# Kernel tuning notes

Measured on AMD Instinct MI355X. Metric: run time of the kernel, lower is better.

The kernel has to match this reference:

```python
import jax, jax.numpy as jnp
import numpy as np

NUM_NODES = 116
EMBED = 64
HIDDEN = 64
OUT_FEAT = 116


def mish(x):
    return x * jnp.tanh(jax.nn.softplus(x))


def sage_conv(x, src, dst, w_l, b_l, w_r, n):
    # PyG SAGEConv (mean aggr): out = lin_l(mean_{j->i} x_j) + lin_r(x_i)
    agg = jax.ops.segment_sum(x[src], dst, num_segments=n)
    cnt = jax.ops.segment_sum(jnp.ones((src.shape[0],), x.dtype), dst, num_segments=n)
    mean = agg / jnp.clip(cnt, 1.0)[:, None]
    return mean @ w_l.T + b_l + x @ w_r.T


def setup_inputs() -> dict:
    key = jax.random.key(0)
    ks = jax.random.split(key, 12)
    B = 64
    N = B * NUM_NODES          # 7424 total nodes
    E = N * 32                 # 237568 edges
    d_in = EMBED * NUM_NODES   # 7424
    d_hid = HIDDEN * NUM_NODES # 7424
    d_out = OUT_FEAT * NUM_NODES  # 13456

    def lin_w(k, fan_out, fan_in):
        s = 1.0 / np.sqrt(fan_in)
        return jax.random.uniform(k, (fan_out, fan_in), jnp.float32, -s, s)

    return {
        "z": jax.random.normal(ks[0], (N, EMBED), jnp.float32),
        "edge_index": jax.random.randint(ks[1], (2, E), 0, N, jnp.int64),
        "batch_size": B,
        "w1_l": lin_w(ks[2], EMBED, EMBED),
        "b1_l": jnp.zeros((EMBED,), jnp.float32),
        "w1_r": lin_w(ks[3], EMBED, EMBED),
        "w2_l": lin_w(ks[4], EMBED, EMBED),
        "b2_l": jnp.zeros((EMBED,), jnp.float32),
        "w2_r": lin_w(ks[5], EMBED, EMBED),
        "fc1_w": lin_w(ks[6], d_hid, d_in),
        "fc1_b": jax.random.uniform(ks[7], (d_hid,), jnp.float32, -1/np.sqrt(d_in), 1/np.sqrt(d_in)),
        "fc2_w": lin_w(ks[8], d_out, d_hid),
        "fc2_b": jax.random.uniform(ks[9], (d_out,), jnp.float32, -1/np.sqrt(d_hid), 1/np.sqrt(d_hid)),
    }


def reference(z, edge_index, batch_size, w1_l, b1_l, w1_r, w2_l, b2_l, w2_r,
              fc1_w, fc1_b, fc2_w, fc2_b):
    n = z.shape[0]
    src, dst = edge_index[0], edge_index[1]
    h = mish(sage_conv(z, src, dst, w1_l, b1_l, w1_r, n))
    h = mish(sage_conv(h, src, dst, w2_l, b2_l, w2_r, n))
    h_flat = h.reshape(batch_size, NUM_NODES * EMBED)
    hidden = mish(h_flat @ fc1_w.T + fc1_b)
    x_rec = (hidden @ fc2_w.T + fc2_b).reshape(batch_size, NUM_NODES, OUT_FEAT)
    # enforce symmetry, unit diagonal
    sym = 0.5 * (x_rec + jnp.swapaxes(x_rec, 1, 2))
    eye = jnp.eye(NUM_NODES, dtype=bool)[None]
    sym = jnp.where(eye, jnp.asarray(1.0, sym.dtype), sym)
    return sym.reshape(batch_size * NUM_NODES, OUT_FEAT)
```

## Files before the change

kernel.cpp:

```cpp
#include <hip/hip_runtime.h>
#include <math.h>

#define NODES_TOT 7424
#define EDGES     237568
#define BATCH     64
#define NN        116
#define KDIM      7424
#define N1        7424
#define N2        13456
#define NKB       116
#define KSPLIT    8

typedef __attribute__((ext_vector_type(8))) short bf16x8;
typedef __attribute__((ext_vector_type(4))) float f32x4;
typedef __attribute__((ext_vector_type(4))) short s16x4;

__device__ __forceinline__ float mish_f(float v) {
    float sp = fmaxf(v, 0.0f) + log1pf(expf(-fabsf(v)));
    return v * tanhf(sp);
}

__device__ __forceinline__ unsigned short bf_rne(float f) {
    unsigned u = __float_as_uint(f);
    u += 0x7fffu + ((u >> 16) & 1u);
    return (unsigned short)(u >> 16);
}

__device__ __forceinline__ void gload_lds16(const void* g, void* l) {
    __builtin_amdgcn_global_load_lds(
        (const __attribute__((address_space(1))) void*)g,
        (__attribute__((address_space(3))) void*)l, 16, 0, 0);
}

__global__ void zero_kernel(int* __restrict__ p, int n) {
    int i = blockIdx.x * 256 + threadIdx.x;
    if (i < n) p[i] = 0;
}

__global__ void hist_kernel(const int* __restrict__ dst, int* __restrict__ hist) {
    int e = blockIdx.x * 256 + threadIdx.x;
    if (e < EDGES) atomicAdd(&hist[dst[e]], 1);
}

__global__ void scan_kernel(const int* __restrict__ hist, int* __restrict__ row_start,
                            int* __restrict__ cursor) {
    __shared__ int s[1024];
    int t = threadIdx.x;
    int base = t * 8;
    int loc[8];
    int sum = 0;
    #pragma unroll
    for (int c = 0; c < 8; ++c) {
        int idx = base + c;
        int v = (idx < NODES_TOT) ? hist[idx] : 0;
        loc[c] = sum;
        sum += v;
    }
    s[t] = sum;
    __syncthreads();
    for (int off = 1; off < 1024; off <<= 1) {
        int v = (t >= off) ? s[t - off] : 0;
        __syncthreads();
        s[t] += v;
        __syncthreads();
    }
    int excl = s[t] - sum;
    #pragma unroll
    for (int c = 0; c < 8; ++c) {
        int idx = base + c;
        if (idx < NODES_TOT) {
            int r = excl + loc[c];
            row_start[idx] = r;
            cursor[idx] = r;
        }
    }
}

__global__ void csr_fill_kernel(const int* __restrict__ src, const int* __restrict__ dst,
                                int* __restrict__ cursor, int* __restrict__ csr_src) {
    int e = blockIdx.x * 256 + threadIdx.x;
    if (e < EDGES) {
        int p = atomicAdd(&cursor[dst[e]], 1);
        csr_src[p] = src[e];
    }
}

template <bool BF>
__global__ void __launch_bounds__(256) conv_kernel(
        const float* __restrict__ x, const int* __restrict__ csr_src,
        const int* __restrict__ row_start, const int* __restrict__ deg_arr,
        const float* __restrict__ w_l, const float* __restrict__ b_l,
        const float* __restrict__ w_r, void* __restrict__ h_out_v) {
    __shared__ float wlT[64 * 64];
    __shared__ float wrT[64 * 64];
    __shared__ float mv[4][64];
    __shared__ float xv[4][64];
    int t = threadIdx.x;
    for (int i = 0; i < 16; ++i) {
        int idx = t + i * 256;
        int f = idx >> 6, k = idx & 63;
        wlT[k * 64 + f] = w_l[idx];
        wrT[k * 64 + f] = w_r[idx];
    }
    int g = t >> 6, f = t & 63;
    __syncthreads();
    for (int nb = blockIdx.x * 4; nb < NODES_TOT; nb += gridDim.x * 4) {
        int node = nb + g;
        int deg = deg_arr[node];
        int rs = row_start[node];
        float sum = 0.f;
        for (int e = 0; e < deg; ++e) {
            int s = csr_src[rs + e];
            sum += x[s * 64 + f];
        }
        float mean = sum / (float)max(deg, 1);
        mv[g][f] = mean;
        xv[g][f] = x[node * 64 + f];
        __syncthreads();
        float o = b_l[f];
        #pragma unroll
        for (int k = 0; k < 64; ++k) {
            o = fmaf(mv[g][k], wlT[k * 64 + f], o);
            o = fmaf(xv[g][k], wrT[k * 64 + f], o);
        }
        float m = mish_f(o);
        if (BF) ((unsigned short*)h_out_v)[node * 64 + f] = bf_rne(m);
        else    ((float*)h_out_v)[node * 64 + f] = m;
        __syncthreads();
    }
}

template <int KS>
__global__ void __launch_bounds__(256) gemm_ring(
        const unsigned short* __restrict__ Abf, const float* __restrict__ W,
        float* __restrict__ Cp, int N) {
    __shared__ __align__(16) float          Wlds[3][4096];
    __shared__ __align__(16) unsigned short Alds[3][4096];
    int t = threadIdx.x;
    int bx = blockIdx.x, by = blockIdx.y;
    int kb0 = (by * NKB) / KS;
    int kb1 = ((by + 1) * NKB) / KS;
    int S = kb1 - kb0;
    int n0 = bx * 64;
    int wv = t >> 6, l = t & 63, l15 = l & 15, hi = l >> 4;

    const float* wsrc[4];
    #pragma unroll
    for (int ii = 0; ii < 4; ++ii) {
        int rloc = wv * 16 + ii * 4 + (l >> 4);
        int wr = n0 + rloc; if (wr >= N) wr = N - 1;
        int g = (l & 15) ^ ((rloc & 7) << 1);
        wsrc[ii] = W + (size_t)wr * KDIM + (size_t)kb0 * 64 + g * 4;
    }
    const unsigned short* asrcp[2];
    #pragma unroll
    for (int ii = 0; ii < 2; ++ii) {
        int rloc = wv * 16 + ii * 8 + (l >> 3);
        int g = (l & 7) ^ (rloc & 7);
        asrcp[ii] = Abf + (size_t)rloc * KDIM + (size_t)kb0 * 64 + g * 8;
    }

    f32x4 acc[4];
    #pragma unroll
    for (int g = 0; g < 4; ++g) acc[g] = (f32x4){0.f, 0.f, 0.f, 0.f};

#define ISSUE(step, buf) do {                                              \
        size_t ko = (size_t)(step) * 64;                                   \
        _Pragma("unroll")                                                  \
        for (int ii = 0; ii < 4; ++ii)                                     \
            gload_lds16(wsrc[ii] + ko, &Wlds[buf][(wv * 16 + ii * 4) * 64]); \
        _Pragma("unroll")                                                  \
        for (int ii = 0; ii < 2; ++ii)                                     \
            gload_lds16(asrcp[ii] + ko, &Alds[buf][(wv * 16 + ii * 8) * 64]); \
    } while (0)

#define MFMAPH(buf) do {                                                   \
        _Pragma("unroll")                                                  \
        for (int s = 0; s < 2; ++s) {                                      \
            int fw = s * 4 + hi;                                           \
            int n = wv * 16 + l15;                                         \
            int g0 = (2 * fw) ^ ((n & 7) << 1);                            \
            f32x4 wlo = *(const f32x4*)&Wlds[buf][n * 64 + g0 * 4];        \
            f32x4 whi = *(const f32x4*)&Wlds[buf][n * 64 + g0 * 4 + 4];    \
            bf16x8 bh;                                                     \
            _Pragma("unroll")                                              \
            for (int j = 0; j < 4; ++j) {                                  \
                bh[j]     = (short)bf_rne(wlo[j]);                         \
                bh[4 + j] = (short)bf_rne(whi[j]);                         \
            }                                                              \
            _Pragma("unroll")                                              \
            for (int g = 0; g < 4; ++g) {                                  \
                int ar = g * 16 + l15;                                     \
                bf16x8 av = *(const bf16x8*)&Alds[buf][ar * 64 + ((fw ^ (ar & 7)) * 8)]; \
                acc[g] = __builtin_amdgcn_mfma_f32_16x16x32_bf16(av, bh, acc[g], 0, 0, 0); \
            }                                                              \
        }                                                                  \
    } while (0)

#define WAIT12() asm volatile("s_waitcnt vmcnt(12)" ::: "memory")
#define WAIT6()  asm volatile("s_waitcnt vmcnt(6)" ::: "memory")
#define WAIT0()  asm volatile("s_waitcnt vmcnt(0)" ::: "memory")
#define RBAR()   asm volatile("s_barrier" ::: "memory")
#define LBAR()   asm volatile("s_waitcnt lgkmcnt(0)\n\ts_barrier" ::: "memory")

    ISSUE(0, 0);
    ISSUE(1, 1);
    ISSUE(2, 2);

    int b = 0;
    for (int s = 0; s < S; ++s) {
        if (s < S - 2) WAIT12();
        else if (s == S - 2) WAIT6();
        else WAIT0();
        RBAR();
        MFMAPH(b);
        LBAR();
        if (s + 3 < S) ISSUE(s + 3, b);
        b = (b == 2) ? 0 : b + 1;
    }

#undef ISSUE
#undef MFMAPH
#undef WAIT12
#undef WAIT6
#undef WAIT0
#undef RBAR
#undef LBAR

    int gn = n0 + wv * 16 + l15;
    if (gn < N) {
        float* cp = Cp + (size_t)by * 64 * N;
        #pragma unroll
        for (int g = 0; g < 4; ++g)
            #pragma unroll
            for (int rr = 0; rr < 4; ++rr)
                cp[(size_t)(g * 16 + hi * 4 + rr) * N + gn] = acc[g][rr];
    }
}

__global__ void reduce1_kernel(const float* __restrict__ Cp, const float* __restrict__ b,
                               unsigned short* __restrict__ A2) {
    int i4 = (blockIdx.x * 256 + threadIdx.x) * 4;
    if (i4 >= BATCH * N1) return;
    int n = i4 % N1;
    f32x4 acc = *(const f32x4*)(b + n);
    #pragma unroll
    for (int s = 0; s < KSPLIT; ++s)
        acc += *(const f32x4*)(Cp + (size_t)s * BATCH * N1 + i4);
    s16x4 o;
    #pragma unroll
    for (int j = 0; j < 4; ++j) o[j] = (short)bf_rne(mish_f(acc[j]));
    *(s16x4*)(A2 + i4) = o;
}

__global__ void reduce2_kernel(const float* __restrict__ Cp, const float* __restrict__ b,
                               float* __restrict__ C2) {
    int i4 = (blockIdx.x * 256 + threadIdx.x) * 4;
    if (i4 >= BATCH * N2) return;
    int n = i4 % N2;
    f32x4 acc = *(const f32x4*)(b + n);
    #pragma unroll
    for (int s = 0; s < KSPLIT; ++s)
        acc += *(const f32x4*)(Cp + (size_t)s * BATCH * N2 + i4);
    *(f32x4*)(C2 + i4) = acc;
}

__global__ void sym_kernel(const float* __restrict__ C2, float* __restrict__ out) {
    int tid = blockIdx.x * 256 + threadIdx.x;
    if (tid >= BATCH * NN * NN) return;
    int j = tid % NN;
    int r = tid / NN;
    int i = r % NN;
    int b = r / NN;
    float v;
    if (i == j) {
        v = 1.0f;
    } else {
        v = 0.5f * (C2[(size_t)b * N2 + i * NN + j] + C2[(size_t)b * N2 + j * NN + i]);
    }
    out[tid] = v;
}

extern "C" void kernel_launch(void* const* d_in, const int* in_sizes, int n_in,
                              void* d_out, int out_size, void* d_ws, size_t ws_size,
                              hipStream_t stream) {
    const float* z     = (const float*)d_in[0];
    const int*   edge  = (const int*)d_in[1];
    const float* w1_l  = (const float*)d_in[3];
    const float* b1_l  = (const float*)d_in[4];
    const float* w1_r  = (const float*)d_in[5];
    const float* w2_l  = (const float*)d_in[6];
    const float* b2_l  = (const float*)d_in[7];
    const float* w2_r  = (const float*)d_in[8];
    const float* fc1_w = (const float*)d_in[9];
    const float* fc1_b = (const float*)d_in[10];
    const float* fc2_w = (const float*)d_in[11];
    const float* fc2_b = (const float*)d_in[12];
    float* out = (float*)d_out;

    char* ws = (char*)d_ws;
    size_t off = 0;
    auto alloc = [&](size_t bytes) {
        void* p = ws + off;
        off = (off + bytes + 255) & ~(size_t)255;
        return p;
    };
    int*            hist      = (int*)alloc(NODES_TOT * 4);
    int*            row_start = (int*)alloc(NODES_TOT * 4);
    int*            cursor    = (int*)alloc(NODES_TOT * 4);
    int*            csr_src   = (int*)alloc((size_t)EDGES * 4);
    float*          h1        = (float*)alloc((size_t)NODES_TOT * 64 * 4);
    unsigned short* A1        = (unsigned short*)alloc((size_t)NODES_TOT * 64 * 2);
    float*          Cp1       = (float*)alloc((size_t)KSPLIT * BATCH * N1 * 4);
    unsigned short* A2        = (unsigned short*)alloc((size_t)BATCH * N1 * 2);
    float*          Cp2       = (float*)alloc((size_t)KSPLIT * BATCH * N2 * 4);
    float*          C2        = (float*)alloc((size_t)BATCH * N2 * 4);

    const int* src = edge;
    const int* dst = edge + EDGES;

    zero_kernel<<<(NODES_TOT + 255) / 256, 256, 0, stream>>>(hist, NODES_TOT);
    hist_kernel<<<(EDGES + 255) / 256, 256, 0, stream>>>(dst, hist);
    scan_kernel<<<1, 1024, 0, stream>>>(hist, row_start, cursor);
    csr_fill_kernel<<<(EDGES + 255) / 256, 256, 0, stream>>>(src, dst, cursor, csr_src);

    conv_kernel<false><<<928, 256, 0, stream>>>(z, csr_src, row_start, hist, w1_l, b1_l, w1_r, h1);
    conv_kernel<true><<<928, 256, 0, stream>>>(h1, csr_src, row_start, hist, w2_l, b2_l, w2_r, A1);

    gemm_ring<KSPLIT><<<dim3(N1 / 64, KSPLIT), 256, 0, stream>>>(A1, fc1_w, Cp1, N1);
    reduce1_kernel<<<(BATCH * N1 / 4 + 255) / 256, 256, 0, stream>>>(Cp1, fc1_b, A2);

    gemm_ring<KSPLIT><<<dim3((N2 + 63) / 64, KSPLIT), 256, 0, stream>>>(A2, fc2_w, Cp2, N2);
    reduce2_kernel<<<(BATCH * N2 / 4 + 255) / 256, 256, 0, stream>>>(Cp2, fc2_b, C2);

    sym_kernel<<<(BATCH * NN * NN + 255) / 256, 256, 0, stream>>>(C2, out);
}
```

Baseline: 332.0 us.

## Fold output symmetrization into fc2 weights and pre-pack GEMM weights to bf16

Because the final symmetrization is linear, fc2's weight rows and biases for each (i,j)/(j,i) pair are averaged into one upper-triangle row. This roughly halves the second GEMM's N dimension, and the sym kernel reads the packed pair result directly. Both fc weight matrices are now converted to bf16 by separate pack kernels on every call. The GEMM then loads bf16 weights with a 128-wide K step and double buffering instead of converting fp32 in the inner loop. The cost is extra memory traffic: the packed bf16 copies are written and read back each call.

```diff
diff --git a/kernel.cpp b/kernel.cpp
--- a/kernel.cpp
+++ b/kernel.cpp
@@ -8,7 +8,9 @@
 #define KDIM      7424
 #define N1        7424
 #define N2        13456
-#define NKB       116
+#define NV        6670
+#define NVP       6720
+#define NKB2      58
 #define KSPLIT    8
 
 typedef __attribute__((ext_vector_type(8))) short bf16x8;
@@ -30,6 +32,10 @@
     __builtin_amdgcn_global_load_lds(
         (const __attribute__((address_space(1))) void*)g,
         (__attribute__((address_space(3))) void*)l, 16, 0, 0);
+}
+
+__device__ __forceinline__ f32x4 ntload4(const float* p) {
+    return __builtin_nontemporal_load((const f32x4*)p);
 }
 
 __global__ void zero_kernel(int* __restrict__ p, int n) {
@@ -130,34 +136,66 @@
     }
 }
 
-template <int KS>
-__global__ void __launch_bounds__(256) gemm_ring(
-        const unsigned short* __restrict__ Abf, const float* __restrict__ W,
-        float* __restrict__ Cp, int N) {
-    __shared__ __align__(16) float          Wlds[3][4096];
-    __shared__ __align__(16) unsigned short Alds[3][4096];
+__global__ void pack1_kernel(const float* __restrict__ W, unsigned short* __restrict__ Wb) {
+    const int total = (N1 * KDIM) / 4;
+    int stride = gridDim.x * 256;
+    for (int i = blockIdx.x * 256 + threadIdx.x; i < total; i += stride) {
+        f32x4 v = ntload4(W + (size_t)i * 4);
+        s16x4 o;
+        #pragma unroll
+        for (int j = 0; j < 4; ++j) o[j] = (short)bf_rne(v[j]);
+        *(s16x4*)(Wb + (size_t)i * 4) = o;
+    }
+}
+
+__global__ void __launch_bounds__(256) pack2_kernel(
+        const float* __restrict__ W, const float* __restrict__ bvec,
+        unsigned short* __restrict__ V, float* __restrict__ bs) {
+    int p = blockIdx.x;
+    int i = 0, rem = p;
+    while (rem >= NN - 1 - i) { rem -= NN - 1 - i; ++i; }
+    int j = i + 1 + rem;
+    const float* r0 = W + (size_t)(i * NN + j) * KDIM;
+    const float* r1 = W + (size_t)(j * NN + i) * KDIM;
+    unsigned short* vp = V + (size_t)p * KDIM;
+    int t = threadIdx.x;
+    #pragma unroll
+    for (int c = 0; c < 8; ++c) {
+        int idx = c * 256 + t;
+        if (idx < KDIM / 4) {
+            f32x4 a = ntload4(r0 + idx * 4);
+            f32x4 b = ntload4(r1 + idx * 4);
+            s16x4 o;
+            #pragma unroll
+            for (int e = 0; e < 4; ++e) o[e] = (short)bf_rne(0.5f * (a[e] + b[e]));
+            *(s16x4*)(vp + idx * 4) = o;
+        }
+    }
+    if (t == 0) bs[p] = 0.5f * (bvec[i * NN + j] + bvec[j * NN + i]);
+}
+
+__global__ void __launch_bounds__(256) gemm_bw(
+        const unsigned short* __restrict__ Abf, const unsigned short* __restrict__ Wb,
+        float* __restrict__ Cp, int N, int NROWS) {
+    __shared__ __align__(16) unsigned short Wlds[2][2][4096];
+    __shared__ __align__(16) unsigned short Alds[2][2][4096];
     int t = threadIdx.x;
     int bx = blockIdx.x, by = blockIdx.y;
-    int kb0 = (by * NKB) / KS;
-    int kb1 = ((by + 1) * NKB) / KS;
+    int kb0 = (by * NKB2) / KSPLIT;
+    int kb1 = ((by + 1) * NKB2) / KSPLIT;
     int S = kb1 - kb0;
     int n0 = bx * 64;
     int wv = t >> 6, l = t & 63, l15 = l & 15, hi = l >> 4;
 
-    const float* wsrc[4];
-    #pragma unroll
-    for (int ii = 0; ii < 4; ++ii) {
-        int rloc = wv * 16 + ii * 4 + (l >> 4);
-        int wr = n0 + rloc; if (wr >= N) wr = N - 1;
-        int g = (l & 15) ^ ((rloc & 7) << 1);
-        wsrc[ii] = W + (size_t)wr * KDIM + (size_t)kb0 * 64 + g * 4;
-    }
+    const unsigned short* wsrcp[2];
     const unsigned short* asrcp[2];
     #pragma unroll
     for (int ii = 0; ii < 2; ++ii) {
         int rloc = wv * 16 + ii * 8 + (l >> 3);
+        int wr = n0 + rloc; if (wr >= NROWS) wr = NROWS - 1;
         int g = (l & 7) ^ (rloc & 7);
-        asrcp[ii] = Abf + (size_t)rloc * KDIM + (size_t)kb0 * 64 + g * 8;
+        wsrcp[ii] = Wb  + (size_t)wr   * KDIM + (size_t)kb0 * 128 + g * 8;
+        asrcp[ii] = Abf + (size_t)rloc * KDIM + (size_t)kb0 * 128 + g * 8;
     }
 
     f32x4 acc[4];
@@ -165,64 +203,57 @@
     for (int g = 0; g < 4; ++g) acc[g] = (f32x4){0.f, 0.f, 0.f, 0.f};
 
 #define ISSUE(step, buf) do {                                              \
-        size_t ko = (size_t)(step) * 64;                                   \
+        size_t ko = (size_t)(step) * 128;                                  \
         _Pragma("unroll")                                                  \
-        for (int ii = 0; ii < 4; ++ii)                                     \
-            gload_lds16(wsrc[ii] + ko, &Wlds[buf][(wv * 16 + ii * 4) * 64]); \
-        _Pragma("unroll")                                                  \
-        for (int ii = 0; ii < 2; ++ii)                                     \
-            gload_lds16(asrcp[ii] + ko, &Alds[buf][(wv * 16 + ii * 8) * 64]); \
-    } while (0)
-
-#define MFMAPH(buf) do {                                                   \
-        _Pragma("unroll")                                                  \
-        for (int s = 0; s < 2; ++s) {                                      \
-            int fw = s * 4 + hi;                                           \
-            int n = wv * 16 + l15;                                         \
-            int g0 = (2 * fw) ^ ((n & 7) << 1);                            \
-            f32x4 wlo = *(const f32x4*)&Wlds[buf][n * 64 + g0 * 4];        \
-            f32x4 whi = *(const f32x4*)&Wlds[buf][n * 64 + g0 * 4 + 4];    \
-            bf16x8 bh;                                                     \
+        for (int h = 0; h < 2; ++h) {                                      \
             _Pragma("unroll")                                              \
-            for (int j = 0; j < 4; ++j) {                                  \
-                bh[j]     = (short)bf_rne(wlo[j]);                         \
-                bh[4 + j] = (short)bf_rne(whi[j]);                         \
-            }                                                              \
-            _Pragma("unroll")                                              \
-            for (int g = 0; g < 4; ++g) {                                  \
-                int ar = g * 16 + l15;                                     \
-                bf16x8 av = *(const bf16x8*)&Alds[buf][ar * 64 + ((fw ^ (ar & 7)) * 8)]; \
-                acc[g] = __builtin_amdgcn_mfma_f32_16x16x32_bf16(av, bh, acc[g], 0, 0, 0); \
+            for (int ii = 0; ii < 2; ++ii) {                               \
+                gload_lds16(wsrcp[ii] + ko + h * 64,                       \
+                            &Wlds[buf][h][(wv * 16 + ii * 8) * 64]);       \
+                gload_lds16(asrcp[ii] + ko + h * 64,                       \
+                            &Alds[buf][h][(wv * 16 + ii * 8) * 64]);       \
             }                                                              \
         }                                                                  \
     } while (0)
 
-#define WAIT12() asm volatile("s_waitcnt vmcnt(12)" ::: "memory")
-#define WAIT6()  asm volatile("s_waitcnt vmcnt(6)" ::: "memory")
+#define MFMAPH(buf) do {                                                   \
+        _Pragma("unroll")                                                  \
+        for (int h = 0; h < 2; ++h) {                                      \
+            _Pragma("unroll")                                              \
+            for (int s = 0; s < 2; ++s) {                                  \
+                int fw = s * 4 + hi;                                       \
+                int n = wv * 16 + l15;                                     \
+                bf16x8 bh = *(const bf16x8*)&Wlds[buf][h][n * 64 + ((fw ^ (n & 7)) * 8)]; \
+                _Pragma("unroll")                                          \
+                for (int g = 0; g < 4; ++g) {                              \
+                    int ar = g * 16 + l15;                                 \
+                    bf16x8 av = *(const bf16x8*)&Alds[buf][h][ar * 64 + ((fw ^ (ar & 7)) * 8)]; \
+                    acc[g] = __builtin_amdgcn_mfma_f32_16x16x32_bf16(av, bh, acc[g], 0, 0, 0); \
+                }                                                          \
+            }                                                              \
+        }                                                                  \
+    } while (0)
+
+#define WAIT8()  asm volatile("s_waitcnt vmcnt(8)" ::: "memory")
 #define WAIT0()  asm volatile("s_waitcnt vmcnt(0)" ::: "memory")
 #define RBAR()   asm volatile("s_barrier" ::: "memory")
 #define LBAR()   asm volatile("s_waitcnt lgkmcnt(0)\n\ts_barrier" ::: "memory")
 
     ISSUE(0, 0);
     ISSUE(1, 1);
-    ISSUE(2, 2);
-
-    int b = 0;
+    int buf = 0;
     for (int s = 0; s < S; ++s) {
-        if (s < S - 2) WAIT12();
-        else if (s == S - 2) WAIT6();
-        else WAIT0();
+        if (s == S - 1) WAIT0(); else WAIT8();
         RBAR();
-        MFMAPH(b);
+        MFMAPH(buf);
         LBAR();
-        if (s + 3 < S) ISSUE(s + 3, b);
-        b = (b == 2) ? 0 : b + 1;
+        if (s + 2 < S) ISSUE(s + 2, buf);
+        buf ^= 1;
     }
 
 #undef ISSUE
 #undef MFMAPH
-#undef WAIT12
-#undef WAIT6
+#undef WAIT8
 #undef WAIT0
 #undef RBAR
 #undef LBAR
@@ -253,19 +284,22 @@
     *(s16x4*)(A2 + i4) = o;
 }
 
-__global__ void reduce2_kernel(const float* __restrict__ Cp, const float* __restrict__ b,
-                               float* __restrict__ C2) {
+__global__ void reduce2_kernel(const float* __restrict__ Cp, const float* __restrict__ bs,
+                               float* __restrict__ C2s) {
     int i4 = (blockIdx.x * 256 + threadIdx.x) * 4;
-    if (i4 >= BATCH * N2) return;
-    int n = i4 % N2;
-    f32x4 acc = *(const f32x4*)(b + n);
+    if (i4 >= BATCH * NVP) return;
+    int n = i4 % NVP;
+    f32x4 acc = {0.f, 0.f, 0.f, 0.f};
     #pragma unroll
     for (int s = 0; s < KSPLIT; ++s)
-        acc += *(const f32x4*)(Cp + (size_t)s * BATCH * N2 + i4);
-    *(f32x4*)(C2 + i4) = acc;
-}
-
-__global__ void sym_kernel(const float* __restrict__ C2, float* __restrict__ out) {
+        acc += *(const f32x4*)(Cp + (size_t)s * BATCH * NVP + i4);
+    #pragma unroll
+    for (int j = 0; j < 4; ++j)
+        if (n + j < NV) acc[j] += bs[n + j];
+    *(f32x4*)(C2s + i4) = acc;
+}
+
+__global__ void sym_kernel(const float* __restrict__ C2s, float* __restrict__ out) {
     int tid = blockIdx.x * 256 + threadIdx.x;
     if (tid >= BATCH * NN * NN) return;
     int j = tid % NN;
@@ -276,7 +310,9 @@
     if (i == j) {
         v = 1.0f;
     } else {
-        v = 0.5f * (C2[(size_t)b * N2 + i * NN + j] + C2[(size_t)b * N2 + j * NN + i]);
+        int lo = min(i, j), hj = max(i, j);
+        int p = lo * (2 * NN - lo - 1) / 2 + (hj - lo - 1);
+        v = C2s[(size_t)b * NVP + p];
     }
     out[tid] = v;
 }
@@ -311,10 +347,13 @@
     int*            csr_src   = (int*)alloc((size_t)EDGES * 4);
     float*          h1        = (float*)alloc((size_t)NODES_TOT * 64 * 4);
     unsigned short* A1        = (unsigned short*)alloc((size_t)NODES_TOT * 64 * 2);
+    unsigned short* W1b       = (unsigned short*)alloc((size_t)N1 * KDIM * 2);
+    unsigned short* Vb        = (unsigned short*)alloc((size_t)NVP * KDIM * 2);
+    float*          bsym      = (float*)alloc((size_t)NV * 4);
     float*          Cp1       = (float*)alloc((size_t)KSPLIT * BATCH * N1 * 4);
     unsigned short* A2        = (unsigned short*)alloc((size_t)BATCH * N1 * 2);
-    float*          Cp2       = (float*)alloc((size_t)KSPLIT * BATCH * N2 * 4);
-    float*          C2        = (float*)alloc((size_t)BATCH * N2 * 4);
+    float*          Cp2       = (float*)alloc((size_t)KSPLIT * BATCH * NVP * 4);
+    float*          C2s       = (float*)alloc((size_t)BATCH * NVP * 4);
 
     const int* src = edge;
     const int* dst = edge + EDGES;
@@ -327,11 +366,13 @@
     conv_kernel<false><<<928, 256, 0, stream>>>(z, csr_src, row_start, hist, w1_l, b1_l, w1_r, h1);
     conv_kernel<true><<<928, 256, 0, stream>>>(h1, csr_src, row_start, hist, w2_l, b2_l, w2_r, A1);
 
-    gemm_ring<KSPLIT><<<dim3(N1 / 64, KSPLIT), 256, 0, stream>>>(A1, fc1_w, Cp1, N1);
+    pack1_kernel<<<2048, 256, 0, stream>>>(fc1_w, W1b);
+    gemm_bw<<<dim3(N1 / 64, KSPLIT), 256, 0, stream>>>(A1, W1b, Cp1, N1, N1);
     reduce1_kernel<<<(BATCH * N1 / 4 + 255) / 256, 256, 0, stream>>>(Cp1, fc1_b, A2);
 
-    gemm_ring<KSPLIT><<<dim3((N2 + 63) / 64, KSPLIT), 256, 0, stream>>>(A2, fc2_w, Cp2, N2);
-    reduce2_kernel<<<(BATCH * N2 / 4 + 255) / 256, 256, 0, stream>>>(Cp2, fc2_b, C2);
-
-    sym_kernel<<<(BATCH * NN * NN + 255) / 256, 256, 0, stream>>>(C2, out);
-}
+    pack2_kernel<<<NV, 256, 0, stream>>>(fc2_w, fc2_b, Vb, bsym);
+    gemm_bw<<<dim3(NVP / 64, KSPLIT), 256, 0, stream>>>(A2, Vb, Cp2, NVP, NV);
+    reduce2_kernel<<<(BATCH * NVP / 4 + 255) / 256, 256, 0, stream>>>(Cp2, bsym, C2s);
+
+    sym_kernel<<<(BATCH * NN * NN + 255) / 256, 256, 0, stream>>>(C2s, out);
+}
```

After: 365.2 us. 10.0% more time.
